# Optimization experiments

Measured on AMD Instinct MI355X. Metric: run time of the kernel, lower is better.

The kernel has to match this reference:

```python
import jax, jax.numpy as jnp
import numpy as np

NUM_TAGS = 5
START_TAG = 3  # ent_to_ix['<START>']
STOP_TAG = 4   # ent_to_ix['<STOP>']
NEG_INF = -10000.0
B, T = 8192, 512


def setup_inputs() -> dict:
    key = jax.random.key(0)
    k1, k2 = jax.random.split(key)
    feats = jax.random.normal(k1, (B, T, NUM_TAGS), dtype=jnp.float32)
    transitions = jax.random.normal(k2, (NUM_TAGS, NUM_TAGS), dtype=jnp.float32)
    # matches __init__: no transition into START, none out of STOP
    transitions = transitions.at[START_TAG, :].set(NEG_INF)
    transitions = transitions.at[:, STOP_TAG].set(NEG_INF)
    return {"feats": feats, "transitions": transitions}


def reference(feats, transitions):
    """Batched CRF forward algorithm (log partition function).

    feats: [B, T, K] emission scores; transitions: [K, K] where
    transitions[next, prev] is the score of prev -> next.
    Returns alpha: [B] log partition per sequence.
    """
    def single(seq):  # seq: [T, K]
        init = jnp.full((NUM_TAGS,), NEG_INF, dtype=seq.dtype).at[START_TAG].set(0.0)

        def step(forward_var, feat):
            # scores[next, prev] = forward_var[prev] + transitions[next, prev] + feat[next]
            scores = forward_var[None, :] + transitions + feat[:, None]
            return jax.nn.logsumexp(scores, axis=1), None

        forward_var, _ = jax.lax.scan(step, init, seq)
        terminal = forward_var + transitions[STOP_TAG]
        return jax.nn.logsumexp(terminal)

    return jax.vmap(single)(feats)
```

## Files before the change

### kernel.cpp

```cpp
#include <hip/hip_runtime.h>

#define BB 8192
#define SEQF 2560

typedef float v2f __attribute__((ext_vector_type(2)));

__device__ __forceinline__ float rfl(float x) {
    return __int_as_float(__builtin_amdgcn_readfirstlane(__float_as_int(x)));
}
__device__ __forceinline__ v2f vsplat(float x) { return (v2f){x, x}; }

__global__ __launch_bounds__(256, 8) void crf_fused(const float* __restrict__ feats,
                                                    const float* __restrict__ trans,
                                                    float* __restrict__ out) {
    const int tid  = threadIdx.x;
    const int lane = tid & 63;
    const int wv   = tid >> 6;
    const int seq  = blockIdx.x * 4 + wv;

    const float4* p = (const float4*)(feats + (size_t)seq * SEQF) + lane * 10;
    float4 q0=p[0], q1=p[1], q2=p[2], q3=p[3], q4=p[4];
    float4 q5=p[5], q6=p[6], q7=p[7], q8=p[8], q9=p[9];
    __builtin_amdgcn_sched_barrier(0);

    const float BIAS = 0.13533528323661270f;
    const float E00=rfl(__expf(trans[0])*BIAS),  E01=rfl(__expf(trans[1])*BIAS),  E02=rfl(__expf(trans[2])*BIAS);
    const float E10=rfl(__expf(trans[5])*BIAS),  E11=rfl(__expf(trans[6])*BIAS),  E12=rfl(__expf(trans[7])*BIAS);
    const float E20=rfl(__expf(trans[10])*BIAS), E21=rfl(__expf(trans[11])*BIAS), E22=rfl(__expf(trans[12])*BIAS);
    const float C0 =rfl(__expf(trans[3])*BIAS),  C1 =rfl(__expf(trans[8])*BIAS),  C2 =rfl(__expf(trans[13])*BIAS);
    const float S0 =rfl(__expf(trans[20])), S1 =rfl(__expf(trans[21])), S2 =rfl(__expf(trans[22]));

    const v2f E00p=vsplat(E00), E01p=vsplat(E01), E02p=vsplat(E02);
    const v2f E10p=vsplat(E10), E11p=vsplat(E11), E12p=vsplat(E12);
    const v2f E20p=vsplat(E20), E21p=vsplat(E21), E22p=vsplat(E22);

    const bool c0 = (lane == 0);
    const v2f GA0 = c0 ? vsplat(C0) : (v2f){E00, E01};
    const v2f GA1 = c0 ? vsplat(C1) : (v2f){E10, E11};
    const v2f GA2 = c0 ? vsplat(C2) : (v2f){E20, E21};
    const float GB0 = c0 ? C0 : E02;
    const float GB1 = c0 ? C1 : E12;
    const float GB2 = c0 ? C2 : E22;

    v2f MA0, MA1, MA2;
    float MB0, MB1, MB2;
    float ls = 0.0f;

#define CRF_STEP(FA, FB, FC) do {                                   \
        float e0 = __expf(FA), e1 = __expf(FB), e2 = __expf(FC);    \
        v2f NA0 = vsplat(e0) * (E00p*MA0 + E01p*MA1 + E02p*MA2);    \
        v2f NA1 = vsplat(e1) * (E10p*MA0 + E11p*MA1 + E12p*MA2);    \
        v2f NA2 = vsplat(e2) * (E20p*MA0 + E21p*MA1 + E22p*MA2);    \
        float NB0 = e0 * (E00*MB0 + E01*MB1 + E02*MB2);             \
        float NB1 = e1 * (E10*MB0 + E11*MB1 + E12*MB2);             \
        float NB2 = e2 * (E20*MB0 + E21*MB1 + E22*MB2);             \
        MA0=NA0; MA1=NA1; MA2=NA2; MB0=NB0; MB1=NB1; MB2=NB2;       \
    } while (0)

#define CRF_RENORM() do {                                           \
        v2f mp = __builtin_elementwise_max(__builtin_elementwise_max(MA0, MA1), MA2); \
        float mm = fmaxf(fmaxf(mp.x, mp.y), fmaxf(fmaxf(MB0, MB1), MB2)); \
        mm = fmaxf(mm, 1e-30f);                                     \
        int ee = (int)((__float_as_uint(mm) >> 23) & 0xffu) - 127;  \
        float sc = __uint_as_float((unsigned)(127 - ee) << 23);     \
        ls += (float)ee;                                            \
        v2f scp = vsplat(sc);                                       \
        MA0*=scp; MA1*=scp; MA2*=scp; MB0*=sc; MB1*=sc; MB2*=sc;    \
    } while (0)

#define TREE_LEVEL(D, RN) do {                                      \
        v2f PA0, PA1, PA2;                                          \
        PA0.x=__shfl_down(MA0.x,D); PA0.y=__shfl_down(MA0.y,D);     \
        PA1.x=__shfl_down(MA1.x,D); PA1.y=__shfl_down(MA1.y,D);     \
        PA2.x=__shfl_down(MA2.x,D); PA2.y=__shfl_down(MA2.y,D);     \
        float PB0=__shfl_down(MB0,D), PB1=__shfl_down(MB1,D), PB2=__shfl_down(MB2,D); \
        float Pls=__shfl_down(ls, D);                               \
        v2f NA0 = vsplat(PA0.x)*MA0 + vsplat(PA0.y)*MA1 + vsplat(PB0)*MA2; \
        v2f NA1 = vsplat(PA1.x)*MA0 + vsplat(PA1.y)*MA1 + vsplat(PB1)*MA2; \
        v2f NA2 = vsplat(PA2.x)*MA0 + vsplat(PA2.y)*MA1 + vsplat(PB2)*MA2; \
        float NB0 = PA0.x*MB0 + PA0.y*MB1 + PB0*MB2;                \
        float NB1 = PA1.x*MB0 + PA1.y*MB1 + PB1*MB2;                \
        float NB2 = PA2.x*MB0 + PA2.y*MB1 + PB2*MB2;                \
        MA0=NA0; MA1=NA1; MA2=NA2; MB0=NB0; MB1=NB1; MB2=NB2;       \
        ls += Pls;                                                  \
        if (RN) CRF_RENORM();                                       \
    } while (0)

    {
        float e0 = __expf(q0.x), e1 = __expf(q0.y), e2 = __expf(q0.z);
        MA0 = vsplat(e0) * GA0;  MB0 = e0 * GB0;
        MA1 = vsplat(e1) * GA1;  MB1 = e1 * GB1;
        MA2 = vsplat(e2) * GA2;  MB2 = e2 * GB2;
    }
    CRF_STEP(q1.y, q1.z, q1.w);
    CRF_STEP(q2.z, q2.w, q3.x);
    CRF_STEP(q3.w, q4.x, q4.y);
    CRF_STEP(q5.x, q5.y, q5.z);
    CRF_STEP(q6.y, q6.z, q6.w);
    CRF_STEP(q7.z, q7.w, q8.x);
    CRF_STEP(q8.w, q9.x, q9.y);
    CRF_RENORM();

    TREE_LEVEL(1, 0);
    TREE_LEVEL(2, 1);
    TREE_LEVEL(4, 0);
    TREE_LEVEL(8, 1);
    TREE_LEVEL(16, 0);
    TREE_LEVEL(32, 1);

    float r = S0*MA0.x + S1*MA1.x + S2*MA2.x;
    float res = __logf(r) + ls * 0.69314718055994531f + 1024.0f;
    if (lane == 0) out[seq] = res;

#undef CRF_STEP
#undef CRF_RENORM
#undef TREE_LEVEL
}

extern "C" void kernel_launch(void* const* d_in, const int* in_sizes, int n_in,
                              void* d_out, int out_size, void* d_ws, size_t ws_size,
                              hipStream_t stream) {
    const float* feats = (const float*)d_in[0];
    const float* trans = (const float*)d_in[1];
    float* out = (float*)d_out;
    (void)d_ws; (void)ws_size;

    crf_fused<<<BB / 4, 256, 0, stream>>>(feats, trans, out);
}
```

Before: 19.22 us.

## Coalesce feature loads across lane quads and redistribute via shuffles

Changes the global load pattern so each group of four lanes reads interleaved float4s. In the old layout each lane read ten contiguous float4s, which strided the wavefront's accesses by 160 bytes; the new layout makes each load instruction more contiguous across the wavefront. Cross-lane shuffles then rebuild each lane's original contiguous chunk before the recurrence. This adds many shuffle instructions and selects, and lowers the launch-bounds occupancy hint from 8 to 6 to leave more registers.

Result: slower. 21.30 us (+10.8%).

```diff
diff --git a/kernel.cpp b/kernel.cpp
--- a/kernel.cpp
+++ b/kernel.cpp
@@ -10,17 +10,22 @@
 }
 __device__ __forceinline__ v2f vsplat(float x) { return (v2f){x, x}; }
 
-__global__ __launch_bounds__(256, 8) void crf_fused(const float* __restrict__ feats,
+__global__ __launch_bounds__(256, 6) void crf_fused(const float* __restrict__ feats,
                                                     const float* __restrict__ trans,
                                                     float* __restrict__ out) {
     const int tid  = threadIdx.x;
     const int lane = tid & 63;
     const int wv   = tid >> 6;
     const int seq  = blockIdx.x * 4 + wv;
+    const int c     = lane & 3;
+    const int qbase = lane & ~3;
+    const bool mybit1 = ((lane >> 1) & 1) != 0;
 
-    const float4* p = (const float4*)(feats + (size_t)seq * SEQF) + lane * 10;
-    float4 q0=p[0], q1=p[1], q2=p[2], q3=p[3], q4=p[4];
-    float4 q5=p[5], q6=p[6], q7=p[7], q8=p[8], q9=p[9];
+    const float4* p4 = (const float4*)(feats + (size_t)seq * SEQF);
+    const int off = (lane >> 2) * 40 + c;
+    float4 r[10];
+    #pragma unroll
+    for (int k = 0; k < 10; ++k) r[k] = p4[off + k * 4];
     __builtin_amdgcn_sched_barrier(0);
 
     const float BIAS = 0.13533528323661270f;
@@ -34,13 +39,28 @@
     const v2f E10p=vsplat(E10), E11p=vsplat(E11), E12p=vsplat(E12);
     const v2f E20p=vsplat(E20), E21p=vsplat(E21), E22p=vsplat(E22);
 
-    const bool c0 = (lane == 0);
-    const v2f GA0 = c0 ? vsplat(C0) : (v2f){E00, E01};
-    const v2f GA1 = c0 ? vsplat(C1) : (v2f){E10, E11};
-    const v2f GA2 = c0 ? vsplat(C2) : (v2f){E20, E21};
-    const float GB0 = c0 ? C0 : E02;
-    const float GB1 = c0 ? C1 : E12;
-    const float GB2 = c0 ? C2 : E22;
+    const bool is0 = (lane == 0);
+    const v2f GA0 = is0 ? vsplat(C0) : (v2f){E00, E01};
+    const v2f GA1 = is0 ? vsplat(C1) : (v2f){E10, E11};
+    const v2f GA2 = is0 ? vsplat(C2) : (v2f){E20, E21};
+    const float GB0 = is0 ? C0 : E02;
+    const float GB1 = is0 ? C1 : E12;
+    const float GB2 = is0 ? C2 : E22;
+
+#define REDIST(J, QD) do {                                              \
+        const int mA0 = (J) >> 2,        mA1 = (10 + (J)) >> 2;         \
+        const int mB0 = (20 + (J)) >> 2, mB1 = (30 + (J)) >> 2;         \
+        const bool hi2 = (((((J) % 4) >> 1)) & 1) != 0;                 \
+        float4 eA = (mybit1 == hi2) ? r[mA0] : r[mA1];                  \
+        float4 eB = (mybit1 == hi2) ? r[mB0] : r[mB1];                  \
+        int src = qbase + ((10 * c + (J)) & 3);                         \
+        float4 gA, gB;                                                  \
+        gA.x = __shfl(eA.x, src); gA.y = __shfl(eA.y, src);             \
+        gA.z = __shfl(eA.z, src); gA.w = __shfl(eA.w, src);             \
+        gB.x = __shfl(eB.x, src); gB.y = __shfl(eB.y, src);             \
+        gB.z = __shfl(eB.z, src); gB.w = __shfl(eB.w, src);             \
+        QD = (c < 2) ? gA : gB;                                         \
+    } while (0)
 
     v2f MA0, MA1, MA2;
     float MB0, MB1, MB2;
@@ -86,18 +106,29 @@
         if (RN) CRF_RENORM();                                       \
     } while (0)
 
+    float4 q0, q1, q2, q3, q4, q5, q6, q7, q8, q9;
+    REDIST(0, q0);
     {
         float e0 = __expf(q0.x), e1 = __expf(q0.y), e2 = __expf(q0.z);
         MA0 = vsplat(e0) * GA0;  MB0 = e0 * GB0;
         MA1 = vsplat(e1) * GA1;  MB1 = e1 * GB1;
         MA2 = vsplat(e2) * GA2;  MB2 = e2 * GB2;
     }
+    REDIST(1, q1);
     CRF_STEP(q1.y, q1.z, q1.w);
+    REDIST(2, q2);
+    REDIST(3, q3);
     CRF_STEP(q2.z, q2.w, q3.x);
+    REDIST(4, q4);
     CRF_STEP(q3.w, q4.x, q4.y);
+    REDIST(5, q5);
     CRF_STEP(q5.x, q5.y, q5.z);
+    REDIST(6, q6);
     CRF_STEP(q6.y, q6.z, q6.w);
+    REDIST(7, q7);
+    REDIST(8, q8);
     CRF_STEP(q7.z, q7.w, q8.x);
+    REDIST(9, q9);
     CRF_STEP(q8.w, q9.x, q9.y);
     CRF_RENORM();
 
@@ -108,10 +139,11 @@
     TREE_LEVEL(16, 0);
     TREE_LEVEL(32, 1);
 
-    float r = S0*MA0.x + S1*MA1.x + S2*MA2.x;
-    float res = __logf(r) + ls * 0.69314718055994531f + 1024.0f;
+    float r_ = S0*MA0.x + S1*MA1.x + S2*MA2.x;
+    float res = __logf(r_) + ls * 0.69314718055994531f + 1024.0f;
     if (lane == 0) out[seq] = res;
 
+#undef REDIST
 #undef CRF_STEP
 #undef CRF_RENORM
 #undef TREE_LEVEL
```
